# Kernel tuning notes

Hardware: AMD Instinct MI355X
Metric: run time of the kernel (lower is better)

## Reference

```python
import jax, jax.numpy as jnp
import numpy as np

TEMP = 0.1   # temperature
EPS = 1e-5   # BatchNorm eps
NEG = -1e9   # mask value for excluded logits

def _conv3x3(x, w):
    return jax.lax.conv_general_dilated(x, w, (1, 1), 'SAME',
                                        dimension_numbers=('NCHW', 'OIHW', 'NCHW'))

def _bn(x, gamma, beta, axes):
    # training-mode BatchNorm2d: stats over `axes` (per-sample (2,3) for the
    # single-sample anchor path, batch (0,2,3) for the dense-key path)
    m = x.mean(axes, keepdims=True)
    v = x.var(axes, keepdims=True)
    return gamma[None, :, None, None] * (x - m) * jax.lax.rsqrt(v + EPS) + beta[None, :, None, None]

def _encode(x, p, axes):
    # GranularityEncoder: conv3x3 -> BN -> ReLU -> conv1x1 -> BN -> ReLU -> GAP
    w1, g1, b1, w2, g2, b2 = p
    h = jax.nn.relu(_bn(_conv3x3(x, w1), g1, b1, axes))
    h = jnp.einsum('nchw,oc->nohw', h, w2)
    h = jax.nn.relu(_bn(h, g2, b2, axes))
    return h.mean((2, 3))  # [N, D]

def _norm(x):
    return x / jnp.maximum(jnp.linalg.norm(x, axis=-1, keepdims=True), 1e-12)

def _loss(sparse, dense, params, decision_mask):
    # Anchors: original encodes one sample at a time -> per-sample BN stats (2,3)
    Q = jnp.stack([_norm(_encode(s, p, (2, 3))) for s, p in zip(sparse, params)])        # [G,cav,D]
    # Dense keys: encoded as a full batch under no_grad -> batch BN stats, stop_gradient
    K = jax.lax.stop_gradient(
        jnp.stack([_norm(_encode(d, p, (0, 2, 3))) for d, p in zip(dense, params)]))     # [G,cav,D]
    S = jnp.einsum('gid,gjd->gij', Q, K)                     # same-granularity sims
    pos = jnp.diagonal(S, axis1=1, axis2=2)                  # [G,cav] l_pos
    cav = S.shape[1]
    S_m = jnp.where(jnp.eye(cav, dtype=bool)[None], NEG, S)  # inter-agent negatives (j != i)
    X = jnp.einsum('gid,hid->gih', Q, K)                     # cross-granularity, same agent
    X_m = jnp.where(jnp.eye(3, dtype=bool)[:, None, :], NEG, X)
    logits = jnp.concatenate([pos[..., None], S_m, X_m], axis=-1) / TEMP  # [G,cav,1+cav+3]
    loss_tab = -logits[..., 0] + jax.nn.logsumexp(logits, axis=-1)        # CE with label 0
    # The per-element loss only depends on (agent, granularity): weight by mask counts.
    cnt = jnp.stack([(decision_mask == g + 1).sum((1, 2)) for g in range(3)]).astype(jnp.float32)  # [G,cav-1]
    cnt = jnp.pad(cnt, ((0, 0), (1, 0)))  # agent 0 is never an anchor (loop starts at i=1)
    tot = cnt.sum()
    return jnp.where(tot > 0, (cnt * loss_tab).sum() / jnp.maximum(tot, 1.0), 0.0)

def setup_inputs():
    key = jax.random.key(0)
    ks = jax.random.split(key, 16)
    CAV, H, W, D = 5, 256, 256, 128
    C = {'g1': 64, 'g2': 32, 'g3': 16}
    inp = {}
    i = 0
    for name, c in C.items():
        inp['sparse_' + name] = jax.random.normal(ks[i], (CAV, c, H, W), jnp.float32); i += 1
        inp['dense_' + name] = jax.random.normal(ks[i], (CAV, c, H, W), jnp.float32); i += 1
        inp['w1_' + name] = jax.random.normal(ks[i], (64, c, 3, 3), jnp.float32) * 0.05; i += 1
        inp['bn1_gamma_' + name] = jnp.ones((64,), jnp.float32)
        inp['bn1_beta_' + name] = jnp.zeros((64,), jnp.float32)
        inp['w2_' + name] = jax.random.normal(ks[i], (D, 64), jnp.float32) * 0.05; i += 1
        inp['bn2_gamma_' + name] = jnp.ones((D,), jnp.float32)
        inp['bn2_beta_' + name] = jnp.zeros((D,), jnp.float32)
    inp['decision_mask'] = jax.random.randint(ks[i], (CAV - 1, 128, 128), 0, 4, jnp.int32)
    return inp

def reference(sparse_g1, dense_g1, w1_g1, bn1_gamma_g1, bn1_beta_g1, w2_g1, bn2_gamma_g1, bn2_beta_g1,
              sparse_g2, dense_g2, w1_g2, bn1_gamma_g2, bn1_beta_g2, w2_g2, bn2_gamma_g2, bn2_beta_g2,
              sparse_g3, dense_g3, w1_g3, bn1_gamma_g3, bn1_beta_g3, w2_g3, bn2_gamma_g3, bn2_beta_g3,
              decision_mask):
    sparse = [sparse_g1, sparse_g2, sparse_g3]
    dense = [dense_g1, dense_g2, dense_g3]
    params = [(w1_g1, bn1_gamma_g1, bn1_beta_g1, w2_g1, bn2_gamma_g1, bn2_beta_g1),
              (w1_g2, bn1_gamma_g2, bn1_beta_g2, w2_g2, bn2_gamma_g2, bn2_beta_g2),
              (w1_g3, bn1_gamma_g3, bn1_beta_g3, w2_g3, bn2_gamma_g3, bn2_beta_g3)]
    return _loss(sparse, dense, params, decision_mask)
```

## Files before the change

kernel.cpp:

```cpp
#include <hip/hip_runtime.h>
#include <math.h>

#define HW 65536
#define NS 5
#define DFEAT 128
#define CMID 64
#define TEMPER 0.1f
#define BNEPS 1e-5f

typedef __attribute__((ext_vector_type(8))) short bf16x8;
typedef __attribute__((ext_vector_type(4))) float f32x4;

__device__ inline short f2bf(float f) {
  union { float f; unsigned u; } v; v.f = f;
  unsigned r = v.u + 0x7fffu + ((v.u >> 16) & 1u);
  return (short)(r >> 16);
}
__device__ inline float bf2f(unsigned short h) {
  union { unsigned u; float f; } v; v.u = ((unsigned)h) << 16;
  return v.f;
}

union U16B { int4 v; unsigned short s[8]; };

__global__ void zero_kernel(float* __restrict__ p, int n) {
  int i = blockIdx.x * blockDim.x + threadIdx.x;
  if (i < n) p[i] = 0.f;
}

template<int C, int CP>
__global__ __launch_bounds__(256) void transpose_kernel(const float* __restrict__ x,
                                                        unsigned short* __restrict__ xT) {
  __shared__ float t[64 * (CP + 1)];
  const int tid = threadIdx.x;
  const int n = blockIdx.y;
  const int pix0 = blockIdx.x * 64;
  const float* xn = x + (size_t)n * C * HW + pix0;
#pragma unroll
  for (int it = 0; it < CP * 64 / 256; ++it) {
    int idx = it * 256 + tid;
    int c = idx >> 6, pix = idx & 63;
    float v = (c < C) ? xn[(size_t)c * HW + pix] : 0.f;
    t[pix * (CP + 1) + c] = v;
  }
  __syncthreads();
  unsigned* out = (unsigned*)(xT + ((size_t)n * HW + pix0) * CP);
#pragma unroll
  for (int it = 0; it < 64 * CP / 2 / 256; ++it) {
    int idx = it * 256 + tid;
    int cp = idx & (CP / 2 - 1), pix = idx / (CP / 2);
    float f0 = t[pix * (CP + 1) + 2 * cp];
    float f1 = t[pix * (CP + 1) + 2 * cp + 1];
    unsigned u = ((unsigned)(unsigned short)f2bf(f0)) |
                 (((unsigned)(unsigned short)f2bf(f1)) << 16);
    out[pix * (CP / 2) + cp] = u;
  }
}

template<int C, int CP>
__global__ void wprep_kernel(const float* __restrict__ w1, const float* __restrict__ w2,
                             unsigned short* __restrict__ w1p, unsigned short* __restrict__ w2p) {
  const int KS = CP / 32;
  const int total1 = 9 * KS * 2 * 64 * 32;
  int idx = blockIdx.x * 256 + threadIdx.x;
  if (idx < total1) {
    int kl = idx & 31; int tmp = idx >> 5;
    int nn = tmp & 63; tmp >>= 6;
    int hl = tmp & 1;  tmp >>= 1;
    int ks = tmp % KS; int s = tmp / KS;
    int ic = ks * 32 + kl;
    float v = (ic < C) ? w1[((size_t)nn * C + ic) * 9 + s] : 0.f;
    short hi = f2bf(v);
    short r = (hl == 0) ? hi : f2bf(v - bf2f((unsigned short)hi));
    w1p[idx] = (unsigned short)r;
  } else if (idx < total1 + 2 * 2 * 128 * 32) {
    int i2 = idx - total1;
    int kl = i2 & 31;
    int nn = (i2 >> 5) & 127;
    int hl = (i2 >> 12) & 1;
    int ks = i2 >> 13;
    float v = w2[nn * 64 + ks * 32 + kl];
    short hi = f2bf(v);
    short r = (hl == 0) ? hi : f2bf(v - bf2f((unsigned short)hi));
    w2p[i2] = (unsigned short)r;
  }
}

template<int CP>
__global__ __launch_bounds__(256, 2) void conv_mfma_kernel(
    const unsigned short* __restrict__ xT,
    const unsigned short* __restrict__ w1p,
    unsigned short* __restrict__ h1,
    float* __restrict__ st)
{
  const int KS = CP / 32;
  constexpr int XSB = 10 * 34 * CP * 2;
  constexpr int HSB = 256 * 72 * 2;
  constexpr int UNI = (XSB > HSB) ? XSB : HSB;
  __shared__ __align__(16) char smem[UNI];
  __shared__ float reds[4][64], redq[4][64];

  const int tid = threadIdx.x;
  const int lane = tid & 63, wave = tid >> 6;
  const int lanen = lane & 15, quad = lane >> 4;
  const int tx = blockIdx.x, ty = blockIdx.y, n = blockIdx.z;
  const int x0 = tx * 32, y0 = ty * 8;

  unsigned short* xs = (unsigned short*)smem;
  const int ROWB = 34 * CP * 2;
  const int xstart = (tx == 0) ? 1 : 0;
  const int xend = (tx == 7) ? 33 : 34;
  for (int r = wave; r < 10; r += 4) {
    int gy = y0 - 1 + r;
    char* rowb = smem + r * ROWB;
    if ((unsigned)gy >= 256u) {
      for (int ofs = lane * 16; ofs < ROWB; ofs += 1024)
        *(int4*)(rowb + ofs) = make_int4(0, 0, 0, 0);
    } else {
      const char* g = (const char*)(xT + ((size_t)n * HW + gy * 256 + x0 - 1 + xstart) * CP);
      int nbytes = (xend - xstart) * CP * 2;
      char* dst = rowb + xstart * CP * 2;
      for (int ofs = lane * 16; ofs < nbytes; ofs += 1024)
        *(int4*)(dst + ofs) = *(const int4*)(g + ofs);
      if (xstart == 1) {
        for (int ofs = lane * 16; ofs < CP * 2; ofs += 1024)
          *(int4*)(rowb + ofs) = make_int4(0, 0, 0, 0);
      }
      if (xend == 33) {
        for (int ofs = lane * 16; ofs < CP * 2; ofs += 1024)
          *(int4*)(rowb + 33 * CP * 2 + ofs) = make_int4(0, 0, 0, 0);
      }
    }
  }
  __syncthreads();

  f32x4 acc[4][4];
#pragma unroll
  for (int t = 0; t < 4; ++t)
#pragma unroll
    for (int nt = 0; nt < 4; ++nt)
      acc[t][nt] = (f32x4){0.f, 0.f, 0.f, 0.f};

  int pbase[4];
#pragma unroll
  for (int t = 0; t < 4; ++t) {
    int p = wave * 64 + t * 16 + lanen;
    pbase[t] = (p >> 5) * 34 + (p & 31);
  }

#pragma unroll
  for (int s = 0; s < 9; ++s) {
    const int dy = s / 3, dx = s % 3;
#pragma unroll
    for (int ks = 0; ks < KS; ++ks) {
      bf16x8 af[4];
#pragma unroll
      for (int t = 0; t < 4; ++t) {
        int eo = (pbase[t] + dy * 34 + dx) * CP + ks * 32 + quad * 8;
        af[t] = *(const bf16x8*)(xs + eo);
      }
#pragma unroll
      for (int hl = 0; hl < 2; ++hl) {
        const unsigned short* wb = w1p + ((((s * KS + ks) * 2 + hl) * 64) + lanen) * 32 + quad * 8;
#pragma unroll
        for (int nt = 0; nt < 4; ++nt) {
          bf16x8 bf = *(const bf16x8*)(wb + nt * 16 * 32);
#pragma unroll
          for (int t = 0; t < 4; ++t)
            acc[t][nt] = __builtin_amdgcn_mfma_f32_16x16x32_bf16(af[t], bf, acc[t][nt], 0, 0, 0);
        }
      }
    }
  }

#pragma unroll
  for (int nt = 0; nt < 4; ++nt) {
    float s = 0.f, q = 0.f;
#pragma unroll
    for (int t = 0; t < 4; ++t)
#pragma unroll
      for (int r = 0; r < 4; ++r) {
        float v = acc[t][nt][r];
        s += v; q += v * v;
      }
    s += __shfl_xor(s, 16); s += __shfl_xor(s, 32);
    q += __shfl_xor(q, 16); q += __shfl_xor(q, 32);
    if (lane < 16) { reds[wave][nt * 16 + lanen] = s; redq[wave][nt * 16 + lanen] = q; }
  }
  __syncthreads();
  if (tid < 64) {
    float s = reds[0][tid] + reds[1][tid] + reds[2][tid] + reds[3][tid];
    float q = redq[0][tid] + redq[1][tid] + redq[2][tid] + redq[3][tid];
    atomicAdd(&st[(n * 64 + tid) * 2 + 0], s);
    atomicAdd(&st[(n * 64 + tid) * 2 + 1], q);
  }

  unsigned short* hs = (unsigned short*)smem;
#pragma unroll
  for (int t = 0; t < 4; ++t)
#pragma unroll
    for (int nt = 0; nt < 4; ++nt)
#pragma unroll
      for (int r = 0; r < 4; ++r) {
        int pix = wave * 64 + t * 16 + quad * 4 + r;
        hs[pix * 72 + nt * 16 + lanen] = (unsigned short)f2bf(acc[t][nt][r]);
      }
  __syncthreads();
#pragma unroll
  for (int it = 0; it < 8; ++it) {
    int idx = it * 256 + tid;
    int ocg = idx & 7, pix = idx >> 3;
    int py = pix >> 5, px = pix & 31;
    int4 v = *(const int4*)(hs + pix * 72 + ocg * 8);
    *(int4*)(h1 + ((size_t)n * HW + (y0 + py) * 256 + x0 + px) * 64 + ocg * 8) = v;
  }
}

__global__ void bn_param_kernel(const float* __restrict__ st,
                                const float* __restrict__ gamma,
                                const float* __restrict__ beta,
                                float* __restrict__ a, float* __restrict__ b,
                                int nch, int batchmode)
{
  int tid = threadIdx.x;
  if (tid >= NS * nch) return;
  int n = tid / nch, ch = tid % nch;
  float s, q, cnt;
  if (batchmode) {
    s = 0.f; q = 0.f;
    for (int m = 0; m < NS; ++m) { s += st[(m * nch + ch) * 2]; q += st[(m * nch + ch) * 2 + 1]; }
    cnt = (float)NS * (float)HW;
  } else {
    s = st[(n * nch + ch) * 2]; q = st[(n * nch + ch) * 2 + 1];
    cnt = (float)HW;
  }
  float mean = s / cnt;
  float var = q / cnt - mean * mean;
  float inv = rsqrtf(var + BNEPS);
  float av = gamma[ch] * inv;
  a[n * nch + ch] = av;
  b[n * nch + ch] = beta[ch] - mean * av;
}

template<bool GAP>
__global__ __launch_bounds__(256, 2) void stage2_mfma_kernel(
    const unsigned short* __restrict__ h1,
    const unsigned short* __restrict__ w2p,
    const float* __restrict__ a1g, const float* __restrict__ b1g,
    const float* __restrict__ a2g, const float* __restrict__ b2g,
    float* __restrict__ out)
{
  __shared__ __align__(16) unsigned short acts[256 * 64];
  __shared__ float red[4][128], redq[4][128];
  const int tid = threadIdx.x;
  const int lane = tid & 63, wave = tid >> 6;
  const int lanen = lane & 15, quad = lane >> 4;
  const int n = blockIdx.y;
  const int pix0 = blockIdx.x * 256;

  const int cg = tid & 7;
  float a1c[8], b1c[8];
#pragma unroll
  for (int j = 0; j < 8; ++j) {
    a1c[j] = a1g[n * 64 + cg * 8 + j];
    b1c[j] = b1g[n * 64 + cg * 8 + j];
  }
  const unsigned short* hb = h1 + ((size_t)n * HW + pix0) * 64;
#pragma unroll
  for (int it = 0; it < 8; ++it) {
    int idx = it * 256 + tid;
    int pix = idx >> 3;
    U16B in, o;
    in.v = *(const int4*)(hb + pix * 64 + cg * 8);
#pragma unroll
    for (int j = 0; j < 8; ++j) {
      float f = bf2f(in.s[j]);
      o.s[j] = (unsigned short)f2bf(fmaxf(a1c[j] * f + b1c[j], 0.f));
    }
    *(int4*)(acts + pix * 64 + cg * 8) = o.v;
  }
  __syncthreads();

  f32x4 acc[4][8];
#pragma unroll
  for (int mt = 0; mt < 4; ++mt)
#pragma unroll
    for (int nt = 0; nt < 8; ++nt)
      acc[mt][nt] = (f32x4){0.f, 0.f, 0.f, 0.f};

#pragma unroll
  for (int ks = 0; ks < 2; ++ks) {
    bf16x8 af[4];
#pragma unroll
    for (int mt = 0; mt < 4; ++mt)
      af[mt] = *(const bf16x8*)(acts + (wave * 64 + mt * 16 + lanen) * 64 + ks * 32 + quad * 8);
#pragma unroll
    for (int hl = 0; hl < 2; ++hl) {
      const unsigned short* wb = w2p + (((ks * 2 + hl) * 128) + lanen) * 32 + quad * 8;
#pragma unroll
      for (int nt = 0; nt < 8; ++nt) {
        bf16x8 bf = *(const bf16x8*)(wb + nt * 16 * 32);
#pragma unroll
        for (int mt = 0; mt < 4; ++mt)
          acc[mt][nt] = __builtin_amdgcn_mfma_f32_16x16x32_bf16(af[mt], bf, acc[mt][nt], 0, 0, 0);
      }
    }
  }

  if constexpr (GAP) {
#pragma unroll
    for (int nt = 0; nt < 8; ++nt) {
      int o = nt * 16 + lanen;
      float a2v = a2g[n * DFEAT + o], b2v = b2g[n * DFEAT + o];
      float s = 0.f;
#pragma unroll
      for (int mt = 0; mt < 4; ++mt)
#pragma unroll
        for (int r = 0; r < 4; ++r)
          s += fmaxf(a2v * acc[mt][nt][r] + b2v, 0.f);
      s += __shfl_xor(s, 16); s += __shfl_xor(s, 32);
      if (lane < 16) red[wave][o] = s;
    }
    __syncthreads();
    if (tid < 128)
      atomicAdd(&out[n * DFEAT + tid], red[0][tid] + red[1][tid] + red[2][tid] + red[3][tid]);
  } else {
#pragma unroll
    for (int nt = 0; nt < 8; ++nt) {
      int o = nt * 16 + lanen;
      float s = 0.f, q = 0.f;
#pragma unroll
      for (int mt = 0; mt < 4; ++mt)
#pragma unroll
        for (int r = 0; r < 4; ++r) {
          float v = acc[mt][nt][r];
          s += v; q += v * v;
        }
      s += __shfl_xor(s, 16); s += __shfl_xor(s, 32);
      q += __shfl_xor(q, 16); q += __shfl_xor(q, 32);
      if (lane < 16) { red[wave][o] = s; redq[wave][o] = q; }
    }
    __syncthreads();
    if (tid < 128) {
      atomicAdd(&out[(n * DFEAT + tid) * 2 + 0], red[0][tid] + red[1][tid] + red[2][tid] + red[3][tid]);
      atomicAdd(&out[(n * DFEAT + tid) * 2 + 1], redq[0][tid] + redq[1][tid] + redq[2][tid] + redq[3][tid]);
    }
  }
}

__global__ void feat_kernel(const float* __restrict__ gap, float* __restrict__ QK) {
  int b = blockIdx.x;
  int e = b / 5, n = b % 5;
  int g = e >> 1, br = e & 1;
  int d = threadIdx.x;
  float v = gap[(e * 5 + n) * DFEAT + d] * (1.0f / (float)HW);
  float q = v * v;
  for (int off = 32; off; off >>= 1) q += __shfl_down(q, off, 64);
  __shared__ float r2[2];
  if ((d & 63) == 0) r2[d >> 6] = q;
  __syncthreads();
  float nrm = sqrtf(r2[0] + r2[1]);
  float inv = 1.0f / fmaxf(nrm, 1e-12f);
  QK[((br * 3 + g) * 5 + n) * DFEAT + d] = v * inv;
}

__global__ __launch_bounds__(256) void loss_kernel(const float* __restrict__ QK,
                                                   const int* __restrict__ dm,
                                                   float* __restrict__ out)
{
  __shared__ float Qs[1920], Ks[1920];
  __shared__ float S[75], X[45], cnt[15], ltab[15];
  const int tid = threadIdx.x;
  for (int i = tid; i < 1920; i += 256) { Qs[i] = QK[i]; Ks[i] = QK[1920 + i]; }
  if (tid < 15) cnt[tid] = 0.f;
  __syncthreads();
  if (tid < 75) {
    int g = tid / 25, i = (tid / 5) % 5, j = tid % 5;
    const float* q = &Qs[(g * 5 + i) * 128];
    const float* k = &Ks[(g * 5 + j) * 128];
    float s = 0.f;
    for (int d = 0; d < 128; ++d) s += q[d] * k[d];
    S[tid] = s;
  } else if (tid < 120) {
    int u = tid - 75;
    int g = u / 15, i = (u % 15) / 3, h = u % 3;
    const float* q = &Qs[(g * 5 + i) * 128];
    const float* k = &Ks[(h * 5 + i) * 128];
    float s = 0.f;
    for (int d = 0; d < 128; ++d) s += q[d] * k[d];
    X[u] = s;
  }
  {
    int a = tid >> 6, l = tid & 63;
    int c0 = 0, c1 = 0, c2 = 0;
    const int* base = dm + a * 16384;
    for (int k = 0; k < 256; ++k) {
      int v = base[k * 64 + l];
      c0 += (v == 1); c1 += (v == 2); c2 += (v == 3);
    }
    atomicAdd(&cnt[0 * 5 + a + 1], (float)c0);
    atomicAdd(&cnt[1 * 5 + a + 1], (float)c1);
    atomicAdd(&cnt[2 * 5 + a + 1], (float)c2);
  }
  __syncthreads();
  if (tid < 15) {
    int g = tid / 5, i = tid % 5;
    const float inv_t = 1.0f / TEMPER;
    float lg[9];
    lg[0] = S[g * 25 + i * 5 + i] * inv_t;
    for (int j = 0; j < 5; ++j) lg[1 + j] = (j == i) ? (-1e9f * inv_t) : S[g * 25 + i * 5 + j] * inv_t;
    for (int h = 0; h < 3; ++h) lg[6 + h] = (h == g) ? (-1e9f * inv_t) : X[g * 15 + i * 3 + h] * inv_t;
    float m = lg[0];
    for (int k = 1; k < 9; ++k) m = fmaxf(m, lg[k]);
    float se = 0.f;
    for (int k = 0; k < 9; ++k) se += expf(lg[k] - m);
    ltab[tid] = -lg[0] + m + logf(se);
  }
  __syncthreads();
  if (tid == 0) {
    float tot = 0.f, acc = 0.f;
    for (int k = 0; k < 15; ++k) { tot += cnt[k]; acc += cnt[k] * ltab[k]; }
    out[0] = (tot > 0.f) ? acc / fmaxf(tot, 1.f) : 0.f;
  }
}

extern "C" void kernel_launch(void* const* d_in, const int* in_sizes, int n_in,
                              void* d_out, int out_size, void* d_ws, size_t ws_size,
                              hipStream_t stream) {
  (void)in_sizes; (void)n_in; (void)out_size; (void)ws_size;

  const float* sp[3]  = {(const float*)d_in[0],  (const float*)d_in[8],  (const float*)d_in[16]};
  const float* dn[3]  = {(const float*)d_in[1],  (const float*)d_in[9],  (const float*)d_in[17]};
  const float* w1[3]  = {(const float*)d_in[2],  (const float*)d_in[10], (const float*)d_in[18]};
  const float* gm1[3] = {(const float*)d_in[3],  (const float*)d_in[11], (const float*)d_in[19]};
  const float* bt1[3] = {(const float*)d_in[4],  (const float*)d_in[12], (const float*)d_in[20]};
  const float* w2[3]  = {(const float*)d_in[5],  (const float*)d_in[13], (const float*)d_in[21]};
  const float* gm2[3] = {(const float*)d_in[6],  (const float*)d_in[14], (const float*)d_in[22]};
  const float* bt2[3] = {(const float*)d_in[7],  (const float*)d_in[15], (const float*)d_in[23]};
  const int*   dm     = (const int*)d_in[24];

  float* ws_f = (float*)d_ws;
  unsigned short* h1u  = (unsigned short*)ws_f;
  unsigned short* xTu  = (unsigned short*)(ws_f + 10485760);
  unsigned short* w1pu = (unsigned short*)(ws_f + 20971520);
  unsigned short* w2pu = (unsigned short*)(ws_f + 20971520 + 36864);
  float* st1 = ws_f + 20971520 + 36864 + 8192;
  float* st2 = st1 + 640;
  float* a1  = st2 + 1280;
  float* b1  = a1 + 320;
  float* a2  = b1 + 320;
  float* b2  = a2 + 640;
  float* gap = b2 + 640;
  float* QK  = gap + 3840;

  zero_kernel<<<15, 256, 0, stream>>>(gap, 3840);

  for (int g = 0; g < 3; ++g) {
    if (g == 0)      wprep_kernel<64, 64><<<(9*2*2*64*32 + 16384 + 255)/256, 256, 0, stream>>>(w1[g], w2[g], w1pu, w2pu);
    else if (g == 1) wprep_kernel<32, 32><<<(9*1*2*64*32 + 16384 + 255)/256, 256, 0, stream>>>(w1[g], w2[g], w1pu, w2pu);
    else             wprep_kernel<16, 32><<<(9*1*2*64*32 + 16384 + 255)/256, 256, 0, stream>>>(w1[g], w2[g], w1pu, w2pu);

    for (int br = 0; br < 2; ++br) {
      const int e = g * 2 + br;
      const float* x = br ? dn[g] : sp[g];

      if (g == 0)      transpose_kernel<64, 64><<<dim3(1024, 5), 256, 0, stream>>>(x, xTu);
      else if (g == 1) transpose_kernel<32, 32><<<dim3(1024, 5), 256, 0, stream>>>(x, xTu);
      else             transpose_kernel<16, 32><<<dim3(1024, 5), 256, 0, stream>>>(x, xTu);

      zero_kernel<<<8, 256, 0, stream>>>(st1, 1920);

      if (g == 0) conv_mfma_kernel<64><<<dim3(8, 32, 5), 256, 0, stream>>>(xTu, w1pu, h1u, st1);
      else        conv_mfma_kernel<32><<<dim3(8, 32, 5), 256, 0, stream>>>(xTu, w1pu, h1u, st1);

      bn_param_kernel<<<1, 320, 0, stream>>>(st1, gm1[g], bt1[g], a1, b1, CMID, br);
      stage2_mfma_kernel<false><<<dim3(256, 5), 256, 0, stream>>>(h1u, w2pu, a1, b1, nullptr, nullptr, st2);
      bn_param_kernel<<<1, 640, 0, stream>>>(st2, gm2[g], bt2[g], a2, b2, DFEAT, br);
      stage2_mfma_kernel<true><<<dim3(256, 5), 256, 0, stream>>>(h1u, w2pu, a1, b1, a2, b2, gap + e * 640);
    }
  }

  feat_kernel<<<30, 128, 0, stream>>>(gap, QK);
  loss_kernel<<<1, 256, 0, stream>>>(QK, dm, (float*)d_out);
}
```

Measured before the change: 1.316 ms.

## Swizzle LDS layouts and fold BN param and zeroing kernels into neighbors

```diff
diff --git a/kernel.cpp b/kernel.cpp
--- a/kernel.cpp
+++ b/kernel.cpp
@@ -8,6 +8,8 @@
 #define TEMPER 0.1f
 #define BNEPS 1e-5f
 
+#define SWZ(a) ((a) ^ ((((a) >> 7) & 7) << 4))
+
 typedef __attribute__((ext_vector_type(8))) short bf16x8;
 typedef __attribute__((ext_vector_type(4))) float f32x4;
 
@@ -30,9 +32,13 @@
 
 template<int C, int CP>
 __global__ __launch_bounds__(256) void transpose_kernel(const float* __restrict__ x,
-                                                        unsigned short* __restrict__ xT) {
+                                                        unsigned short* __restrict__ xT,
+                                                        float* __restrict__ st) {
   __shared__ float t[64 * (CP + 1)];
   const int tid = threadIdx.x;
+  if (blockIdx.x == 0 && blockIdx.y == 0) {
+    for (int i = tid; i < 1920; i += 256) st[i] = 0.f;
+  }
   const int n = blockIdx.y;
   const int pix0 = blockIdx.x * 64;
   const float* xn = x + (size_t)n * C * HW + pix0;
@@ -95,7 +101,7 @@
 {
   const int KS = CP / 32;
   constexpr int XSB = 10 * 34 * CP * 2;
-  constexpr int HSB = 256 * 72 * 2;
+  constexpr int HSB = 256 * 64 * 2;
   constexpr int UNI = (XSB > HSB) ? XSB : HSB;
   __shared__ __align__(16) char smem[UNI];
   __shared__ float reds[4][64], redq[4][64];
@@ -106,29 +112,36 @@
   const int tx = blockIdx.x, ty = blockIdx.y, n = blockIdx.z;
   const int x0 = tx * 32, y0 = ty * 8;
 
-  unsigned short* xs = (unsigned short*)smem;
   const int ROWB = 34 * CP * 2;
   const int xstart = (tx == 0) ? 1 : 0;
   const int xend = (tx == 7) ? 33 : 34;
   for (int r = wave; r < 10; r += 4) {
     int gy = y0 - 1 + r;
-    char* rowb = smem + r * ROWB;
+    const int rowbase = r * ROWB;
     if ((unsigned)gy >= 256u) {
-      for (int ofs = lane * 16; ofs < ROWB; ofs += 1024)
-        *(int4*)(rowb + ofs) = make_int4(0, 0, 0, 0);
+      for (int ofs = lane * 16; ofs < ROWB; ofs += 1024) {
+        int la = rowbase + ofs;
+        *(int4*)(smem + SWZ(la)) = make_int4(0, 0, 0, 0);
+      }
     } else {
       const char* g = (const char*)(xT + ((size_t)n * HW + gy * 256 + x0 - 1 + xstart) * CP);
       int nbytes = (xend - xstart) * CP * 2;
-      char* dst = rowb + xstart * CP * 2;
-      for (int ofs = lane * 16; ofs < nbytes; ofs += 1024)
-        *(int4*)(dst + ofs) = *(const int4*)(g + ofs);
+      int dst0 = rowbase + xstart * CP * 2;
+      for (int ofs = lane * 16; ofs < nbytes; ofs += 1024) {
+        int la = dst0 + ofs;
+        *(int4*)(smem + SWZ(la)) = *(const int4*)(g + ofs);
+      }
       if (xstart == 1) {
-        for (int ofs = lane * 16; ofs < CP * 2; ofs += 1024)
-          *(int4*)(rowb + ofs) = make_int4(0, 0, 0, 0);
+        for (int ofs = lane * 16; ofs < CP * 2; ofs += 1024) {
+          int la = rowbase + ofs;
+          *(int4*)(smem + SWZ(la)) = make_int4(0, 0, 0, 0);
+        }
       }
       if (xend == 33) {
-        for (int ofs = lane * 16; ofs < CP * 2; ofs += 1024)
-          *(int4*)(rowb + 33 * CP * 2 + ofs) = make_int4(0, 0, 0, 0);
+        for (int ofs = lane * 16; ofs < CP * 2; ofs += 1024) {
+          int la = rowbase + 33 * CP * 2 + ofs;
+          *(int4*)(smem + SWZ(la)) = make_int4(0, 0, 0, 0);
+        }
       }
     }
   }
@@ -156,8 +169,8 @@
       bf16x8 af[4];
 #pragma unroll
       for (int t = 0; t < 4; ++t) {
-        int eo = (pbase[t] + dy * 34 + dx) * CP + ks * 32 + quad * 8;
-        af[t] = *(const bf16x8*)(xs + eo);
+        int la = (pbase[t] + dy * 34 + dx) * (CP * 2) + ks * 64 + quad * 16;
+        af[t] = *(const bf16x8*)(smem + SWZ(la));
       }
 #pragma unroll
       for (int hl = 0; hl < 2; ++hl) {
@@ -195,7 +208,6 @@
     atomicAdd(&st[(n * 64 + tid) * 2 + 1], q);
   }
 
-  unsigned short* hs = (unsigned short*)smem;
 #pragma unroll
   for (int t = 0; t < 4; ++t)
 #pragma unroll
@@ -203,7 +215,8 @@
 #pragma unroll
       for (int r = 0; r < 4; ++r) {
         int pix = wave * 64 + t * 16 + quad * 4 + r;
-        hs[pix * 72 + nt * 16 + lanen] = (unsigned short)f2bf(acc[t][nt][r]);
+        int la = pix * 128 + (nt * 16 + lanen) * 2;
+        *(unsigned short*)(smem + SWZ(la)) = (unsigned short)f2bf(acc[t][nt][r]);
       }
   __syncthreads();
 #pragma unroll
@@ -211,20 +224,15 @@
     int idx = it * 256 + tid;
     int ocg = idx & 7, pix = idx >> 3;
     int py = pix >> 5, px = pix & 31;
-    int4 v = *(const int4*)(hs + pix * 72 + ocg * 8);
+    int la = pix * 128 + ocg * 16;
+    int4 v = *(const int4*)(smem + SWZ(la));
     *(int4*)(h1 + ((size_t)n * HW + (y0 + py) * 256 + x0 + px) * 64 + ocg * 8) = v;
   }
 }
 
-__global__ void bn_param_kernel(const float* __restrict__ st,
-                                const float* __restrict__ gamma,
-                                const float* __restrict__ beta,
-                                float* __restrict__ a, float* __restrict__ b,
-                                int nch, int batchmode)
-{
-  int tid = threadIdx.x;
-  if (tid >= NS * nch) return;
-  int n = tid / nch, ch = tid % nch;
+__device__ inline void bn_pair(const float* __restrict__ st, const float* __restrict__ gamma,
+                               const float* __restrict__ beta, int nch, int n, int ch,
+                               int batchmode, float& a, float& b) {
   float s, q, cnt;
   if (batchmode) {
     s = 0.f; q = 0.f;
@@ -237,33 +245,49 @@
   float mean = s / cnt;
   float var = q / cnt - mean * mean;
   float inv = rsqrtf(var + BNEPS);
-  float av = gamma[ch] * inv;
-  a[n * nch + ch] = av;
-  b[n * nch + ch] = beta[ch] - mean * av;
+  a = gamma[ch] * inv;
+  b = beta[ch] - mean * a;
 }
 
 template<bool GAP>
 __global__ __launch_bounds__(256, 2) void stage2_mfma_kernel(
     const unsigned short* __restrict__ h1,
     const unsigned short* __restrict__ w2p,
-    const float* __restrict__ a1g, const float* __restrict__ b1g,
-    const float* __restrict__ a2g, const float* __restrict__ b2g,
+    const float* __restrict__ st1, const float* __restrict__ gm1, const float* __restrict__ bt1,
+    const float* __restrict__ st2, const float* __restrict__ gm2, const float* __restrict__ bt2,
+    int batchmode,
     float* __restrict__ out)
 {
-  __shared__ __align__(16) unsigned short acts[256 * 64];
+  __shared__ __align__(16) char acts[256 * 64 * 2];
   __shared__ float red[4][128], redq[4][128];
+  __shared__ float s_a1[64], s_b1[64], s_a2[128], s_b2[128];
   const int tid = threadIdx.x;
   const int lane = tid & 63, wave = tid >> 6;
   const int lanen = lane & 15, quad = lane >> 4;
   const int n = blockIdx.y;
   const int pix0 = blockIdx.x * 256;
 
+  if (tid < 64) {
+    float a, b;
+    bn_pair(st1, gm1, bt1, CMID, n, tid, batchmode, a, b);
+    s_a1[tid] = a; s_b1[tid] = b;
+  }
+  if constexpr (GAP) {
+    if (tid >= 64 && tid < 192) {
+      int ch = tid - 64;
+      float a, b;
+      bn_pair(st2, gm2, bt2, DFEAT, n, ch, batchmode, a, b);
+      s_a2[ch] = a; s_b2[ch] = b;
+    }
+  }
+  __syncthreads();
+
   const int cg = tid & 7;
   float a1c[8], b1c[8];
 #pragma unroll
   for (int j = 0; j < 8; ++j) {
-    a1c[j] = a1g[n * 64 + cg * 8 + j];
-    b1c[j] = b1g[n * 64 + cg * 8 + j];
+    a1c[j] = s_a1[cg * 8 + j];
+    b1c[j] = s_b1[cg * 8 + j];
   }
   const unsigned short* hb = h1 + ((size_t)n * HW + pix0) * 64;
 #pragma unroll
@@ -277,7 +301,8 @@
       float f = bf2f(in.s[j]);
       o.s[j] = (unsigned short)f2bf(fmaxf(a1c[j] * f + b1c[j], 0.f));
     }
-    *(int4*)(acts + pix * 64 + cg * 8) = o.v;
+    int la = pix * 128 + cg * 16;
+    *(int4*)(acts + SWZ(la)) = o.v;
   }
   __syncthreads();
 
@@ -292,8 +317,10 @@
   for (int ks = 0; ks < 2; ++ks) {
     bf16x8 af[4];
 #pragma unroll
-    for (int mt = 0; mt < 4; ++mt)
-      af[mt] = *(const bf16x8*)(acts + (wave * 64 + mt * 16 + lanen) * 64 + ks * 32 + quad * 8);
+    for (int mt = 0; mt < 4; ++mt) {
+      int la = (wave * 64 + mt * 16 + lanen) * 128 + ks * 64 + quad * 16;
+      af[mt] = *(const bf16x8*)(acts + SWZ(la));
+    }
 #pragma unroll
     for (int hl = 0; hl < 2; ++hl) {
       const unsigned short* wb = w2p + (((ks * 2 + hl) * 128) + lanen) * 32 + quad * 8;
@@ -311,7 +338,7 @@
 #pragma unroll
     for (int nt = 0; nt < 8; ++nt) {
       int o = nt * 16 + lanen;
-      float a2v = a2g[n * DFEAT + o], b2v = b2g[n * DFEAT + o];
+      float a2v = s_a2[o], b2v = s_b2[o];
       float s = 0.f;
 #pragma unroll
       for (int mt = 0; mt < 4; ++mt)
@@ -446,11 +473,7 @@
   unsigned short* w2pu = (unsigned short*)(ws_f + 20971520 + 36864);
   float* st1 = ws_f + 20971520 + 36864 + 8192;
   float* st2 = st1 + 640;
-  float* a1  = st2 + 1280;
-  float* b1  = a1 + 320;
-  float* a2  = b1 + 320;
-  float* b2  = a2 + 640;
-  float* gap = b2 + 640;
+  float* gap = st2 + 1280;
   float* QK  = gap + 3840;
 
   zero_kernel<<<15, 256, 0, stream>>>(gap, 3840);
@@ -464,19 +487,17 @@
       const int e = g * 2 + br;
       const float* x = br ? dn[g] : sp[g];
 
-      if (g == 0)      transpose_kernel<64, 64><<<dim3(1024, 5), 256, 0, stream>>>(x, xTu);
-      else if (g == 1) transpose_kernel<32, 32><<<dim3(1024, 5), 256, 0, stream>>>(x, xTu);
-      else             transpose_kernel<16, 32><<<dim3(1024, 5), 256, 0, stream>>>(x, xTu);
-
-      zero_kernel<<<8, 256, 0, stream>>>(st1, 1920);
+      if (g == 0)      transpose_kernel<64, 64><<<dim3(1024, 5), 256, 0, stream>>>(x, xTu, st1);
+      else if (g == 1) transpose_kernel<32, 32><<<dim3(1024, 5), 256, 0, stream>>>(x, xTu, st1);
+      else             transpose_kernel<16, 32><<<dim3(1024, 5), 256, 0, stream>>>(x, xTu, st1);
 
       if (g == 0) conv_mfma_kernel<64><<<dim3(8, 32, 5), 256, 0, stream>>>(xTu, w1pu, h1u, st1);
       else        conv_mfma_kernel<32><<<dim3(8, 32, 5), 256, 0, stream>>>(xTu, w1pu, h1u, st1);
 
-      bn_param_kernel<<<1, 320, 0, stream>>>(st1, gm1[g], bt1[g], a1, b1, CMID, br);
-      stage2_mfma_kernel<false><<<dim3(256, 5), 256, 0, stream>>>(h1u, w2pu, a1, b1, nullptr, nullptr, st2);
-      bn_param_kernel<<<1, 640, 0, stream>>>(st2, gm2[g], bt2[g], a2, b2, DFEAT, br);
-      stage2_mfma_kernel<true><<<dim3(256, 5), 256, 0, stream>>>(h1u, w2pu, a1, b1, a2, b2, gap + e * 640);
+      stage2_mfma_kernel<false><<<dim3(256, 5), 256, 0, stream>>>(
+          h1u, w2pu, st1, gm1[g], bt1[g], nullptr, nullptr, nullptr, br, st2);
+      stage2_mfma_kernel<true><<<dim3(256, 5), 256, 0, stream>>>(
+          h1u, w2pu, st1, gm1[g], bt1[g], st2, gm2[g], bt2[g], br, gap + e * 640);
     }
   }
 
```

New measurement: 1.284 ms. 2.4% less time.
